# Kernel optimization log

Hardware: AMD Instinct MI355X
Metric: run time of the kernel (lower is better)

## Reference

```python
import jax, jax.numpy as jnp
import numpy as np

BN_EPS = 1e-3
NUM_HEADS = 4
HEAD_CH = 16  # embed_channels // num_heads = 64 // 4


def _conv_bn(x, w, g, b, rm, rv, pad):
    # Conv2d (no bias) followed by eval-mode BatchNorm2d, activation=Identity.
    y = jax.lax.conv_general_dilated(
        x, w, window_strides=(1, 1), padding=[(pad, pad), (pad, pad)],
        dimension_numbers=("NCHW", "OIHW", "NCHW"))
    s = g * jax.lax.rsqrt(rv + BN_EPS)
    return y * s[None, :, None, None] + (b - rm * s)[None, :, None, None]


def setup_inputs() -> dict:
    key = jax.random.key(0)
    ks = jax.random.split(key, 16)
    B, Cin, H, W = 8, 128, 160, 160
    N, Cg, Ce, Co = 80, 512, 64, 128
    x = jax.random.normal(ks[0], (B, Cin, H, W), jnp.float32)
    guide = jax.random.normal(ks[1], (B, N, Cg), jnp.float32)
    # embed_conv (1x1) + BN params
    w_embed = jax.random.normal(ks[2], (Ce, Cin, 1, 1), jnp.float32) * 0.05
    g1 = jnp.ones((Ce,), jnp.float32)
    b1 = jnp.zeros((Ce,), jnp.float32)
    rm1 = jax.random.normal(ks[3], (Ce,), jnp.float32) * 0.1
    rv1 = jax.random.uniform(ks[4], (Ce,), jnp.float32) + 0.5
    # guide_fc
    Wg = jax.random.normal(ks[5], (Ce, Cg), jnp.float32) * 0.02
    bg = jnp.zeros((Ce,), jnp.float32)
    # per-head bias
    attn_bias = jnp.zeros((NUM_HEADS,), jnp.float32)
    # project_conv (3x3) + BN params
    w_proj = jax.random.normal(ks[6], (Co, Cin, 3, 3), jnp.float32) * 0.02
    g2 = jnp.ones((Co,), jnp.float32)
    b2 = jnp.zeros((Co,), jnp.float32)
    rm2 = jax.random.normal(ks[7], (Co,), jnp.float32) * 0.1
    rv2 = jax.random.uniform(ks[8], (Co,), jnp.float32) + 0.5
    return {"x": x, "guide": guide, "w_embed": w_embed, "g1": g1, "b1": b1,
            "rm1": rm1, "rv1": rv1, "Wg": Wg, "bg": bg, "attn_bias": attn_bias,
            "w_proj": w_proj, "g2": g2, "b2": b2, "rm2": rm2, "rv2": rv2}


def reference(x, guide, w_embed, g1, b1, rm1, rv1, Wg, bg, attn_bias,
              w_proj, g2, b2, rm2, rv2):
    B, _, H, W = x.shape
    nh, hc = NUM_HEADS, HEAD_CH
    # guide_fc -> [B, N, nh, hc]
    g = (jnp.einsum("bnc,ec->bne", guide, Wg) + bg).reshape(B, -1, nh, hc)
    # embed_conv (1x1, BN, no act) -> [B, nh, hc, H, W]
    e = _conv_bn(x, w_embed, g1, b1, rm1, rv1, 0).reshape(B, nh, hc, H, W)
    # attn: dot over head channels, max over N guides, scale, bias, sigmoid
    aw = jnp.einsum("bmchw,bnmc->bmhwn", e, g)  # [B, nh, H, W, N]
    aw = jnp.max(aw, axis=-1) * (1.0 / np.sqrt(hc)) + attn_bias[None, :, None, None]
    aw = jax.nn.sigmoid(aw)  # scale == 1.0 (with_scale=False)
    # project_conv (3x3, BN, no act), gate per-head, merge heads
    xp = _conv_bn(x, w_proj, g2, b2, rm2, rv2, 1).reshape(B, nh, -1, H, W)
    return (xp * aw[:, :, None]).reshape(B, -1, H, W)
```

## Files before the change

### kernel.cpp

```cpp
#include <hip/hip_runtime.h>
#include <hip/hip_bf16.h>
#include <stdint.h>


typedef __attribute__((ext_vector_type(8))) short short8;
typedef __attribute__((ext_vector_type(4))) float f32x4;

#define PCH2 ((size_t)8 * 162 * 176 * 32)

#define GLDS(gp, lp) __builtin_amdgcn_global_load_lds(                         \
    (const __attribute__((address_space(1))) void*)(gp),                       \
    (__attribute__((address_space(3))) void*)(lp), 16, 0, 0)

__device__ __forceinline__ unsigned short f2bf(float f) {
  unsigned int u = __float_as_uint(f);
  u += 0x7fff + ((u >> 16) & 1);
  return (unsigned short)(u >> 16);
}

__global__ __launch_bounds__(256) void k_prep_x(const float* __restrict__ x,
                                                unsigned short* __restrict__ P2) {
  __shared__ unsigned short T[8192];
  int b = blockIdx.x / 112, blk = blockIdx.x % 112;
  int tid = threadIdx.x;
  int px = blk * 256 + tid;
  int hp = px / 176, wp = px - hp * 176;
  bool interior = (px < 28512) && (hp >= 1) && (hp <= 160) && (wp >= 8) && (wp < 168);
  const float* xb = x + (size_t)b * 128 * 25600 + (hp - 1) * 160 + (wp - 8);
  int q = tid >> 2, os = tid & 3;

  for (int cs = 0; cs < 4; ++cs) {
    short8 v[4];
#pragma unroll
    for (int s = 0; s < 4; ++s) {
#pragma unroll
      for (int j = 0; j < 8; ++j) {
        float f = interior ? xb[(size_t)(cs * 32 + s * 8 + j) * 25600] : 0.f;
        v[s][j] = (short)f2bf(f);
      }
    }
    if (cs) __syncthreads();
#pragma unroll
    for (int s = 0; s < 4; ++s)
      *(short8*)(&T[(tid * 4 + (s ^ (tid & 3))) * 8]) = v[s];
    __syncthreads();
#pragma unroll
    for (int ph = 0; ph < 4; ++ph) {
      int lpx = ph * 64 + q;
      int opx = blk * 256 + lpx;
      if (opx < 28512) {
        int ohp = opx / 176, owp = opx - ohp * 176;
        size_t obase = (((size_t)b * 162 + ohp) * 176 + owp) * 32 + os * 8;
        short8 w = *(const short8*)(&T[(lpx * 4 + (os ^ (lpx & 3))) * 8]);
        *(short8*)(&P2[(size_t)cs * PCH2 + obase]) = w;
      }
    }
  }
}

__global__ __launch_bounds__(256) void k_prep_misc(
    const float* __restrict__ w_embed, const float* __restrict__ w_proj,
    const float* __restrict__ g2, const float* __restrict__ b2,
    const float* __restrict__ rm2, const float* __restrict__ rv2,
    unsigned short* __restrict__ W1t, unsigned short* __restrict__ Wpt,
    float* __restrict__ s2, float* __restrict__ t2) {
  int idx = blockIdx.x * 256 + threadIdx.x;
  if (idx < 8192) { W1t[idx] = f2bf(w_embed[idx]); return; }
  idx -= 8192;
  if (idx < 147456) {
    int cs = idx / 36864, r = idx - cs * 36864;
    int tap = r >> 12, r2 = r & 4095;
    int co = r2 >> 5, ci5 = r2 & 31;
    int ci = cs * 32 + ci5;
    Wpt[idx] = f2bf(w_proj[(co * 128 + ci) * 9 + tap]);
    return;
  }
  idx -= 147456;
  if (idx < 128) {
    float s = g2[idx] * rsqrtf(rv2[idx] + 1e-3f);
    s2[idx] = s;
    t2[idx] = b2[idx] - rm2[idx] * s;
  }
}

__global__ __launch_bounds__(64) void k_guide(
    const float* __restrict__ guide, const float* __restrict__ Wg,
    const float* __restrict__ bg, const float* __restrict__ g1,
    const float* __restrict__ b1, const float* __restrict__ rm1,
    const float* __restrict__ rv1, unsigned short* __restrict__ Gpad,
    float* __restrict__ Cst) {
  int b = blockIdx.x / 80, n = blockIdx.x % 80;
  __shared__ float gs[512];
  const float* gr = guide + ((size_t)b * 80 + n) * 512;
  for (int i = threadIdx.x; i < 512; i += 64) gs[i] = gr[i];
  __syncthreads();
  int ce = threadIdx.x;
  const float* wr = Wg + (size_t)ce * 512;
  float acc = 0.f;
  for (int k = 0; k < 512; k += 4)
    acc += gs[k] * wr[k] + gs[k + 1] * wr[k + 1] + gs[k + 2] * wr[k + 2] +
           gs[k + 3] * wr[k + 3];
  float raw = acc + bg[ce];
  float s1 = g1[ce] * rsqrtf(rv1[ce] + 1e-3f);
  float t1 = b1[ce] - rm1[ce] * s1;
  int head = ce >> 4, c = ce & 15;
  size_t gp = (((size_t)b * 4 + head) * 80 + n) * 32;
  Gpad[gp + c] = f2bf(raw * s1);
  Gpad[gp + 16 + c] = 0;
  float cp = raw * t1;
  cp += __shfl_xor(cp, 1);
  cp += __shfl_xor(cp, 2);
  cp += __shfl_xor(cp, 4);
  cp += __shfl_xor(cp, 8);
  if (c == 0) Cst[((size_t)b * 4 + head) * 80 + n] = cp;
}

__global__ __launch_bounds__(256, 3) void k_mega(
    const unsigned short* __restrict__ P2, const unsigned short* __restrict__ W1t,
    const unsigned short* __restrict__ Wpt, const unsigned short* __restrict__ Gpad,
    const float* __restrict__ Cst, const float* __restrict__ attn_bias,
    const float* __restrict__ s2, const float* __restrict__ t2,
    float* __restrict__ out) {
  __shared__ unsigned short XA[2][7680];
  int b = blockIdx.x & 7;
  int r = blockIdx.x >> 3;
  int blkN = r & 1;
  int tile = r >> 1;
  int ht = tile / 5, wt = tile - ht * 5;
  int h0 = ht * 4, w0 = wt * 32;
  int tid = threadIdx.x, lane = tid & 63, wv = tid >> 6;
  int l15 = lane & 15, l4 = lane >> 4;
  int mh = wv >> 1, nh = wv & 1;

  size_t aoff[4];
#pragma unroll
  for (int k = 0; k < 4; ++k) {
    int i = wv * 4 + k;
    int c = i * 64 + lane;
    int cc = (c < 960) ? c : 0;
    int row = cc / 160, rem = cc - row * 160;
    int px = rem >> 2, sp = rem & 3;
    int s = sp ^ ((px >> 1) & 3);
    aoff[k] = (((size_t)b * 162 + h0 + row) * 176 + (w0 + 7 + px)) * 32 + s * 8;
  }
  int abase[2][3];
#pragma unroll
  for (int wh = 0; wh < 2; ++wh)
#pragma unroll
    for (int kx = 0; kx < 3; ++kx) {
      int px = wh * 16 + l15 + kx;
      abase[wh][kx] = px * 4 + (l4 ^ ((px >> 1) & 3));
    }
  int boff2[2];
#pragma unroll
  for (int nt = 0; nt < 2; ++nt)
    boff2[nt] = (blkN * 64 + nh * 32 + nt * 16 + l15) * 32 + l4 * 8;

  f32x4 acc[4][2], accE[4];
#pragma unroll
  for (int j = 0; j < 4; ++j) {
    acc[j][0] = (f32x4){0.f, 0.f, 0.f, 0.f};
    acc[j][1] = (f32x4){0.f, 0.f, 0.f, 0.f};
    accE[j]   = (f32x4){0.f, 0.f, 0.f, 0.f};
  }

#pragma unroll
  for (int k = 0; k < 4; ++k) {
    int i = wv * 4 + k;
    if (i < 15) GLDS(P2 + aoff[k], &XA[0][i * 512]);
  }
  short8 Bb[3][2];
#pragma unroll
  for (int nt = 0; nt < 2; ++nt) {
    Bb[0][nt] = *(const short8*)(Wpt + boff2[nt]);
    Bb[1][nt] = *(const short8*)(Wpt + 4096 + boff2[nt]);
  }
  __syncthreads();

#pragma unroll
  for (int cs = 0; cs < 4; ++cs) {
    if (cs < 3) {
#pragma unroll
      for (int k = 0; k < 4; ++k) {
        int i = wv * 4 + k;
        if (i < 15)
          GLDS(P2 + (size_t)(cs + 1) * PCH2 + aoff[k], &XA[(cs + 1) & 1][i * 512]);
      }
    }
#pragma unroll
    for (int tap = 0; tap < 9; ++tap) {
      const int t = cs * 9 + tap;
      if (t + 2 < 36) {
#pragma unroll
        for (int nt = 0; nt < 2; ++nt)
          Bb[(t + 2) % 3][nt] =
              *(const short8*)(Wpt + (size_t)(t + 2) * 4096 + boff2[nt]);
      }
      int ky = tap / 3, kx = tap - ky * 3;
      short8 A[4];
#pragma unroll
      for (int j = 0; j < 4; ++j) {
        int rr = mh * 2 + (j >> 1) + ky;
        A[j] = *(const short8*)(&XA[cs & 1][(rr * 160 + abase[j & 1][kx]) * 8]);
      }
      if (tap == 4) {
        short8 BE = *(const short8*)(W1t + (blkN * 32 + nh * 16 + l15) * 128 +
                                     cs * 32 + l4 * 8);
#pragma unroll
        for (int j = 0; j < 4; ++j)
          accE[j] = __builtin_amdgcn_mfma_f32_16x16x32_bf16(A[j], BE, accE[j], 0, 0, 0);
      }
#pragma unroll
      for (int j = 0; j < 4; ++j)
#pragma unroll
        for (int nt = 0; nt < 2; ++nt)
          acc[j][nt] = __builtin_amdgcn_mfma_f32_16x16x32_bf16(
              A[j], Bb[t % 3][nt], acc[j][nt], 0, 0, 0);
    }
    if (cs < 3) __syncthreads();
  }
  __syncthreads();

  unsigned short* Eb = &XA[0][0];
  float* AWLf = (float*)(&XA[0][0] + 4096);
#pragma unroll
  for (int j = 0; j < 4; ++j)
#pragma unroll
    for (int rr = 0; rr < 4; ++rr) {
      int pxl = (j >> 1) * 32 + (j & 1) * 16 + l4 * 4 + rr;
      int chunk = (l15 >> 3) ^ (pxl & 1);
      Eb[wv * 1024 + pxl * 16 + chunk * 8 + (l15 & 7)] = f2bf(accE[j][rr]);
    }

  const f32x4 zf = (f32x4){0.f, 0.f, 0.f, 0.f};
  int head = blkN * 2 + nh;
  short8 Ga[5];
  f32x4 cst[5];
#pragma unroll
  for (int m5 = 0; m5 < 5; ++m5) {
    Ga[m5] = *(const short8*)(Gpad + (((size_t)b * 4 + head) * 80 + m5 * 16 + l15) * 32 + l4 * 8);
    cst[m5] = *(const f32x4*)(Cst + ((size_t)b * 4 + head) * 80 + m5 * 16 + l4 * 4);
  }
  float bias = attn_bias[head];
#pragma unroll
  for (int nt = 0; nt < 4; ++nt) {
    int pxl = nt * 16 + l15;
    int chr = (l4 & 1) ^ (pxl & 1);
    short8 Bf = *(const short8*)(&Eb[wv * 1024 + pxl * 16 + chr * 8]);
    float mx = -3.0e38f;
#pragma unroll
    for (int m5 = 0; m5 < 5; ++m5) {
      f32x4 s = __builtin_amdgcn_mfma_f32_16x16x32_bf16(Ga[m5], Bf, zf, 0, 0, 0);
#pragma unroll
      for (int rr = 0; rr < 4; ++rr) mx = fmaxf(mx, s[rr] + cst[m5][rr]);
    }
    mx = fmaxf(mx, __shfl_xor(mx, 16));
    mx = fmaxf(mx, __shfl_xor(mx, 32));
    if (lane < 16) AWLf[wv * 64 + nt * 16 + lane] = 1.f / (1.f + __expf(-(mx * 0.25f + bias)));
  }

  float s2v[2], t2v[2];
#pragma unroll
  for (int nt = 0; nt < 2; ++nt) {
    int co = blkN * 64 + nh * 32 + nt * 16 + l15;
    s2v[nt] = s2[co];
    t2v[nt] = t2[co];
  }
#pragma unroll
  for (int j = 0; j < 4; ++j) {
    int h = h0 + mh * 2 + (j >> 1);
    int wbase = w0 + (j & 1) * 16 + l4 * 4;
    int pb = (j >> 1) * 32 + (j & 1) * 16 + l4 * 4;
    f32x4 a0 = *(const f32x4*)(&AWLf[wv * 64 + pb]);
#pragma unroll
    for (int nt = 0; nt < 2; ++nt) {
      int co = blkN * 64 + nh * 32 + nt * 16 + l15;
      f32x4 o;
#pragma unroll
      for (int rr = 0; rr < 4; ++rr) o[rr] = (acc[j][nt][rr] * s2v[nt] + t2v[nt]) * a0[rr];
      *(f32x4*)(out + (size_t)(b * 128 + co) * 25600 + h * 160 + wbase) = o;
    }
  }
}

extern "C" void kernel_launch(void* const* d_in, const int* in_sizes, int n_in,
                              void* d_out, int out_size, void* d_ws, size_t ws_size,
                              hipStream_t stream) {
  (void)in_sizes; (void)n_in; (void)out_size; (void)ws_size;
  const float* x         = (const float*)d_in[0];
  const float* guide     = (const float*)d_in[1];
  const float* w_embed   = (const float*)d_in[2];
  const float* g1        = (const float*)d_in[3];
  const float* b1        = (const float*)d_in[4];
  const float* rm1       = (const float*)d_in[5];
  const float* rv1       = (const float*)d_in[6];
  const float* Wg        = (const float*)d_in[7];
  const float* bg        = (const float*)d_in[8];
  const float* attn_bias = (const float*)d_in[9];
  const float* w_proj    = (const float*)d_in[10];
  const float* g2        = (const float*)d_in[11];
  const float* b2        = (const float*)d_in[12];
  const float* rm2       = (const float*)d_in[13];
  const float* rv2       = (const float*)d_in[14];
  float* out = (float*)d_out;

  char* ws = (char*)d_ws;
  unsigned short* P2   = (unsigned short*)(ws);
  unsigned short* W1t  = (unsigned short*)(ws + 58392576);
  unsigned short* Wpt  = (unsigned short*)(ws + 58408960);
  unsigned short* Gpad = (unsigned short*)(ws + 58703872);
  float* Cst           = (float*)(ws + 58867712);
  float* s2            = (float*)(ws + 58877952);
  float* t2            = (float*)(ws + 58878464);

  k_prep_x<<<8 * 112, 256, 0, stream>>>(x, P2);
  k_prep_misc<<<609, 256, 0, stream>>>(w_embed, w_proj, g2, b2, rm2, rv2, W1t, Wpt, s2, t2);
  k_guide<<<640, 64, 0, stream>>>(guide, Wg, bg, g1, b1, rm1, rv1, Gpad, Cst);
  k_mega<<<3200, 256, 0, stream>>>(P2, W1t, Wpt, Gpad, Cst, attn_bias, s2, t2, out);
}
```

Measured before the change: 142.0 us.

## Remap warp tiling to one row per wave with all 64 output channels

Result: slower. 207.9 us (+46.5%).

```diff
diff --git a/kernel.cpp b/kernel.cpp
--- a/kernel.cpp
+++ b/kernel.cpp
@@ -130,7 +130,6 @@
   int h0 = ht * 4, w0 = wt * 32;
   int tid = threadIdx.x, lane = tid & 63, wv = tid >> 6;
   int l15 = lane & 15, l4 = lane >> 4;
-  int mh = wv >> 1, nh = wv & 1;
 
   size_t aoff[4];
 #pragma unroll
@@ -151,17 +150,18 @@
       int px = wh * 16 + l15 + kx;
       abase[wh][kx] = px * 4 + (l4 ^ ((px >> 1) & 3));
     }
-  int boff2[2];
-#pragma unroll
-  for (int nt = 0; nt < 2; ++nt)
-    boff2[nt] = (blkN * 64 + nh * 32 + nt * 16 + l15) * 32 + l4 * 8;
-
-  f32x4 acc[4][2], accE[4];
-#pragma unroll
-  for (int j = 0; j < 4; ++j) {
-    acc[j][0] = (f32x4){0.f, 0.f, 0.f, 0.f};
-    acc[j][1] = (f32x4){0.f, 0.f, 0.f, 0.f};
-    accE[j]   = (f32x4){0.f, 0.f, 0.f, 0.f};
+  int boff[4];
+#pragma unroll
+  for (int nt = 0; nt < 4; ++nt)
+    boff[nt] = (blkN * 64 + nt * 16 + l15) * 32 + l4 * 8;
+
+  f32x4 acc[2][4], accE[2][2];
+#pragma unroll
+  for (int wh = 0; wh < 2; ++wh) {
+#pragma unroll
+    for (int nt = 0; nt < 4; ++nt) acc[wh][nt] = (f32x4){0.f, 0.f, 0.f, 0.f};
+#pragma unroll
+    for (int he = 0; he < 2; ++he) accE[wh][he] = (f32x4){0.f, 0.f, 0.f, 0.f};
   }
 
 #pragma unroll
@@ -169,11 +169,11 @@
     int i = wv * 4 + k;
     if (i < 15) GLDS(P2 + aoff[k], &XA[0][i * 512]);
   }
-  short8 Bb[3][2];
-#pragma unroll
-  for (int nt = 0; nt < 2; ++nt) {
-    Bb[0][nt] = *(const short8*)(Wpt + boff2[nt]);
-    Bb[1][nt] = *(const short8*)(Wpt + 4096 + boff2[nt]);
+  short8 Bb[3][4];
+#pragma unroll
+  for (int nt = 0; nt < 4; ++nt) {
+    Bb[0][nt] = *(const short8*)(Wpt + boff[nt]);
+    Bb[1][nt] = *(const short8*)(Wpt + 4096 + boff[nt]);
   }
   __syncthreads();
 
@@ -192,30 +192,33 @@
       const int t = cs * 9 + tap;
       if (t + 2 < 36) {
 #pragma unroll
-        for (int nt = 0; nt < 2; ++nt)
+        for (int nt = 0; nt < 4; ++nt)
           Bb[(t + 2) % 3][nt] =
-              *(const short8*)(Wpt + (size_t)(t + 2) * 4096 + boff2[nt]);
+              *(const short8*)(Wpt + (size_t)(t + 2) * 4096 + boff[nt]);
       }
       int ky = tap / 3, kx = tap - ky * 3;
-      short8 A[4];
-#pragma unroll
-      for (int j = 0; j < 4; ++j) {
-        int rr = mh * 2 + (j >> 1) + ky;
-        A[j] = *(const short8*)(&XA[cs & 1][(rr * 160 + abase[j & 1][kx]) * 8]);
-      }
+      int rr = wv + ky;
+      short8 A[2];
+#pragma unroll
+      for (int wh = 0; wh < 2; ++wh)
+        A[wh] = *(const short8*)(&XA[cs & 1][(rr * 160 + abase[wh][kx]) * 8]);
       if (tap == 4) {
-        short8 BE = *(const short8*)(W1t + (blkN * 32 + nh * 16 + l15) * 128 +
-                                     cs * 32 + l4 * 8);
-#pragma unroll
-        for (int j = 0; j < 4; ++j)
-          accE[j] = __builtin_amdgcn_mfma_f32_16x16x32_bf16(A[j], BE, accE[j], 0, 0, 0);
-      }
-#pragma unroll
-      for (int j = 0; j < 4; ++j)
-#pragma unroll
-        for (int nt = 0; nt < 2; ++nt)
-          acc[j][nt] = __builtin_amdgcn_mfma_f32_16x16x32_bf16(
-              A[j], Bb[t % 3][nt], acc[j][nt], 0, 0, 0);
+#pragma unroll
+        for (int he = 0; he < 2; ++he) {
+          short8 BE = *(const short8*)(W1t + (blkN * 32 + he * 16 + l15) * 128 +
+                                       cs * 32 + l4 * 8);
+#pragma unroll
+          for (int wh = 0; wh < 2; ++wh)
+            accE[wh][he] = __builtin_amdgcn_mfma_f32_16x16x32_bf16(
+                A[wh], BE, accE[wh][he], 0, 0, 0);
+        }
+      }
+#pragma unroll
+      for (int wh = 0; wh < 2; ++wh)
+#pragma unroll
+        for (int nt = 0; nt < 4; ++nt)
+          acc[wh][nt] = __builtin_amdgcn_mfma_f32_16x16x32_bf16(
+              A[wh], Bb[t % 3][nt], acc[wh][nt], 0, 0, 0);
     }
     if (cs < 3) __syncthreads();
   }
@@ -224,60 +227,69 @@
   unsigned short* Eb = &XA[0][0];
   float* AWLf = (float*)(&XA[0][0] + 4096);
 #pragma unroll
-  for (int j = 0; j < 4; ++j)
-#pragma unroll
-    for (int rr = 0; rr < 4; ++rr) {
-      int pxl = (j >> 1) * 32 + (j & 1) * 16 + l4 * 4 + rr;
-      int chunk = (l15 >> 3) ^ (pxl & 1);
-      Eb[wv * 1024 + pxl * 16 + chunk * 8 + (l15 & 7)] = f2bf(accE[j][rr]);
-    }
+  for (int wh = 0; wh < 2; ++wh)
+#pragma unroll
+    for (int he = 0; he < 2; ++he)
+#pragma unroll
+      for (int rr = 0; rr < 4; ++rr) {
+        int px = wh * 16 + l4 * 4 + rr;
+        int ce = he * 16 + l15;
+        int chk = (ce >> 3) ^ (px & 3);
+        Eb[wv * 1024 + px * 32 + chk * 8 + (ce & 7)] = f2bf(accE[wh][he][rr]);
+      }
 
   const f32x4 zf = (f32x4){0.f, 0.f, 0.f, 0.f};
-  int head = blkN * 2 + nh;
-  short8 Ga[5];
-  f32x4 cst[5];
-#pragma unroll
-  for (int m5 = 0; m5 < 5; ++m5) {
-    Ga[m5] = *(const short8*)(Gpad + (((size_t)b * 4 + head) * 80 + m5 * 16 + l15) * 32 + l4 * 8);
-    cst[m5] = *(const f32x4*)(Cst + ((size_t)b * 4 + head) * 80 + m5 * 16 + l4 * 4);
-  }
-  float bias = attn_bias[head];
+#pragma unroll
+  for (int he = 0; he < 2; ++he) {
+    int head = blkN * 2 + he;
+    short8 Ga[5];
+    f32x4 cst[5];
+#pragma unroll
+    for (int m5 = 0; m5 < 5; ++m5) {
+      Ga[m5] = *(const short8*)(Gpad + (((size_t)b * 4 + head) * 80 + m5 * 16 + l15) * 32 + l4 * 8);
+      cst[m5] = *(const f32x4*)(Cst + ((size_t)b * 4 + head) * 80 + m5 * 16 + l4 * 4);
+    }
+    float bias = attn_bias[head];
+#pragma unroll
+    for (int pxg = 0; pxg < 2; ++pxg) {
+      int px = pxg * 16 + l15;
+      int chk = ((he * 2 + (l4 & 1)) ^ (px & 3));
+      short8 Bf = *(const short8*)(&Eb[wv * 1024 + px * 32 + chk * 8]);
+      float mx = -3.0e38f;
+#pragma unroll
+      for (int m5 = 0; m5 < 5; ++m5) {
+        f32x4 s = __builtin_amdgcn_mfma_f32_16x16x32_bf16(Ga[m5], Bf, zf, 0, 0, 0);
+#pragma unroll
+        for (int rr = 0; rr < 4; ++rr) mx = fmaxf(mx, s[rr] + cst[m5][rr]);
+      }
+      mx = fmaxf(mx, __shfl_xor(mx, 16));
+      mx = fmaxf(mx, __shfl_xor(mx, 32));
+      if (lane < 16)
+        AWLf[(wv * 2 + he) * 32 + pxg * 16 + lane] =
+            1.f / (1.f + __expf(-(mx * 0.25f + bias)));
+    }
+  }
+
+  float s2v[4], t2v[4];
 #pragma unroll
   for (int nt = 0; nt < 4; ++nt) {
-    int pxl = nt * 16 + l15;
-    int chr = (l4 & 1) ^ (pxl & 1);
-    short8 Bf = *(const short8*)(&Eb[wv * 1024 + pxl * 16 + chr * 8]);
-    float mx = -3.0e38f;
-#pragma unroll
-    for (int m5 = 0; m5 < 5; ++m5) {
-      f32x4 s = __builtin_amdgcn_mfma_f32_16x16x32_bf16(Ga[m5], Bf, zf, 0, 0, 0);
-#pragma unroll
-      for (int rr = 0; rr < 4; ++rr) mx = fmaxf(mx, s[rr] + cst[m5][rr]);
-    }
-    mx = fmaxf(mx, __shfl_xor(mx, 16));
-    mx = fmaxf(mx, __shfl_xor(mx, 32));
-    if (lane < 16) AWLf[wv * 64 + nt * 16 + lane] = 1.f / (1.f + __expf(-(mx * 0.25f + bias)));
-  }
-
-  float s2v[2], t2v[2];
-#pragma unroll
-  for (int nt = 0; nt < 2; ++nt) {
-    int co = blkN * 64 + nh * 32 + nt * 16 + l15;
+    int co = blkN * 64 + nt * 16 + l15;
     s2v[nt] = s2[co];
     t2v[nt] = t2[co];
   }
-#pragma unroll
-  for (int j = 0; j < 4; ++j) {
-    int h = h0 + mh * 2 + (j >> 1);
-    int wbase = w0 + (j & 1) * 16 + l4 * 4;
-    int pb = (j >> 1) * 32 + (j & 1) * 16 + l4 * 4;
-    f32x4 a0 = *(const f32x4*)(&AWLf[wv * 64 + pb]);
-#pragma unroll
-    for (int nt = 0; nt < 2; ++nt) {
-      int co = blkN * 64 + nh * 32 + nt * 16 + l15;
+  int h = h0 + wv;
+#pragma unroll
+  for (int wh = 0; wh < 2; ++wh) {
+    int wbase = w0 + wh * 16 + l4 * 4;
+    f32x4 a0 = *(const f32x4*)(&AWLf[(wv * 2 + 0) * 32 + wh * 16 + l4 * 4]);
+    f32x4 a1 = *(const f32x4*)(&AWLf[(wv * 2 + 1) * 32 + wh * 16 + l4 * 4]);
+#pragma unroll
+    for (int nt = 0; nt < 4; ++nt) {
+      int co = blkN * 64 + nt * 16 + l15;
+      f32x4 g = (nt >> 1) ? a1 : a0;
       f32x4 o;
 #pragma unroll
-      for (int rr = 0; rr < 4; ++rr) o[rr] = (acc[j][nt][rr] * s2v[nt] + t2v[nt]) * a0[rr];
+      for (int rr = 0; rr < 4; ++rr) o[rr] = (acc[wh][nt][rr] * s2v[nt] + t2v[nt]) * g[rr];
       *(f32x4*)(out + (size_t)(b * 128 + co) * 25600 + h * 160 + wbase) = o;
     }
   }
```
